# Optimization experiments

Hardware: AMD Instinct MI355X
Metric: run time of the kernel (lower is better)

Reference implementation:

```python
import jax, jax.numpy as jnp
import numpy as np

EMBED = 128          # embed_dim
HID = 128            # hidden_dim (must equal embed_dim for the view math to work)
HEADS = 4
HEAD_DIM = EMBED // HEADS  # = HID // HEADS = 32
N = 50000            # source cells
M = 50000            # target cells
E = 400000           # edges (nnz of inter_neighborhood)


def setup_inputs() -> dict:
    key = jax.random.key(0)
    ks = jax.random.split(key, 13)
    s = lambda d: 1.0 / np.sqrt(d)
    return {
        "source_features": jax.random.normal(ks[0], (N, EMBED), jnp.float32),
        "target_features": jax.random.normal(ks[1], (M, EMBED), jnp.float32),
        "edge_targets": jax.random.randint(ks[2], (E,), 0, M, dtype=jnp.int32),
        "edge_sources": jax.random.randint(ks[3], (E,), 0, N, dtype=jnp.int32),
        "Ws": jax.random.normal(ks[4], (EMBED, HEADS * HID), jnp.float32) * s(EMBED),
        "bs": jnp.zeros((HEADS * HID,), jnp.float32),
        "Wt": jax.random.normal(ks[5], (EMBED, HEADS * HID), jnp.float32) * s(EMBED),
        "bt": jnp.zeros((HEADS * HID,), jnp.float32),
        "attn_w": jax.random.normal(ks[6], (HEADS, HID), jnp.float32),
        "Wm": jax.random.normal(ks[7], (EMBED, EMBED), jnp.float32) * s(EMBED),
        "bm": jnp.zeros((EMBED,), jnp.float32),
        "Wo": jax.random.normal(ks[8], (EMBED, EMBED), jnp.float32) * s(EMBED),
        "bo": jnp.zeros((EMBED,), jnp.float32),
    }


def reference(source_features, target_features, edge_targets, edge_sources,
              Ws, bs, Wt, bt, attn_w, Wm, bm, Wo, bo):
    # Gather endpoint features per edge: [E, EMBED]
    src = source_features[edge_sources]
    tgt = target_features[edge_targets]
    # Fused linear + GELU attention hidden: [E, HEADS, HID]
    hidden = jax.nn.gelu((src @ Ws + bs) + (tgt @ Wt + bt), approximate=False)
    hidden = hidden.reshape(E, HEADS, HID)
    # Attention logits per edge/head: [E, HEADS]
    logits = jnp.einsum('ehd,hd->eh', hidden, attn_w)
    # Scatter-softmax over edges sharing the same target node
    mx = jax.ops.segment_max(logits, edge_targets, num_segments=M)
    ex = jnp.exp(logits - mx[edge_targets])
    den = jax.ops.segment_sum(ex, edge_targets, num_segments=M)
    scores = ex / den[edge_targets]                      # [E, HEADS]
    # Messages: [E, HEADS, HEAD_DIM], weighted and scatter-summed to targets
    msgs = (src @ Wm + bm).reshape(E, HEADS, HEAD_DIM) * scores[..., None]
    agg = jax.ops.segment_sum(msgs, edge_targets, num_segments=M)
    agg = agg.reshape(M, HEADS * HEAD_DIM)               # [M, EMBED]
    return agg @ Wo + bo
```

## Files before the change

### kernel.cpp

```cpp
#include <hip/hip_runtime.h>
#include <math.h>


typedef __bf16 bf16x8 __attribute__((ext_vector_type(8)));
typedef float  f32x4  __attribute__((ext_vector_type(4)));
typedef float  f32x2  __attribute__((ext_vector_type(2)));

__device__ __forceinline__ unsigned short f2bf(float x) {
    unsigned u = __float_as_uint(x);
    u += 0x7FFFu + ((u >> 16) & 1u);
    return (unsigned short)(u >> 16);
}
__device__ __forceinline__ float bf2f(unsigned short b) {
    return __uint_as_float(((unsigned)b) << 16);
}
__device__ __forceinline__ unsigned pack_tr(float a, float b) {
    return (__float_as_uint(a) >> 16) | (__float_as_uint(b) & 0xFFFF0000u);
}
__device__ __forceinline__ float res16(float x) {
    return x - __uint_as_float(__float_as_uint(x) & 0xFFFF0000u);
}
__device__ __forceinline__ unsigned short bf_rn(float x) {
    return (unsigned short)((__float_as_uint(x) + 0x8000u) >> 16);
}
__device__ __forceinline__ f32x2 up2(unsigned u) {
    f32x2 r;
    r.x = __uint_as_float(u << 16);
    r.y = __uint_as_float(u & 0xFFFF0000u);
    return r;
}
__device__ __forceinline__ float exp2_fast(float x) {
#if __has_builtin(__builtin_amdgcn_exp2f)
    return __builtin_amdgcn_exp2f(x);
#else
    return exp2f(x);
#endif
}

__device__ __forceinline__ f32x2 gelu2(f32x2 v) {
    f32x2 v2 = v * v;
    f32x2 u  = v * (v2 * 0.10294355f + 2.30220820f);
    f32x2 e;
    e.x = exp2_fast(u.x);
    e.y = exp2_fast(u.y);
    f32x2 r;
    r.x = __builtin_amdgcn_rcpf(e.x + 1.0f);
    r.y = __builtin_amdgcn_rcpf(e.y + 1.0f);
    return v - v * r;
}

__device__ __forceinline__ float edge_logit(uint4 h,
    f32x2 ht0, f32x2 ht1, f32x2 ht2, f32x2 ht3,
    f32x2 aw0, f32x2 aw1, f32x2 aw2, f32x2 aw3) {
    f32x2 qv = gelu2(up2(h.x) + ht0) * aw0;
    qv += gelu2(up2(h.y) + ht1) * aw1;
    qv += gelu2(up2(h.z) + ht2) * aw2;
    qv += gelu2(up2(h.w) + ht3) * aw3;
    return qv.x + qv.y;
}

__global__ __launch_bounds__(128)
void prep_weights_kernel(const float* __restrict__ Ws, const float* __restrict__ Wm,
                         const float* __restrict__ Wt, const float* __restrict__ Wo,
                         const float* __restrict__ bs, const float* __restrict__ bm,
                         unsigned short* __restrict__ WThi, unsigned short* __restrict__ WTlo,
                         float* __restrict__ bias_cat) {
    int n = blockIdx.x, k = threadIdx.x;
    float w;
    if      (n < 512)  w = Ws[(size_t)k * 512 + n];
    else if (n < 640)  w = Wm[(size_t)k * 128 + (n - 512)];
    else if (n < 1152) w = Wt[(size_t)k * 512 + (n - 640)];
    else               w = Wo[(size_t)k * 128 + (n - 1152)];
    unsigned short hi = f2bf(w);
    WThi[(size_t)n * 128 + k] = hi;
    WTlo[(size_t)n * 128 + k] = f2bf(w - bf2f(hi));
    if (k == 0 && n < 640) bias_cat[n] = (n < 512) ? bs[n] : bm[n - 512];
}

__global__ void hist_kernel(const int* __restrict__ tgt, int* __restrict__ counts, int E) {
    int e = blockIdx.x * blockDim.x + threadIdx.x;
    if (e < E) atomicAdd(&counts[tgt[e]], 1);
}

__global__ __launch_bounds__(256)
void scan_partial_kernel(const int* __restrict__ counts, int* __restrict__ partials, int M) {
    __shared__ int sdata[256];
    int b = blockIdx.x, tid = threadIdx.x;
    int base = b * 1024 + tid * 4;
    int s = 0;
#pragma unroll
    for (int k = 0; k < 4; ++k) { int idx = base + k; if (idx < M) s += counts[idx]; }
    sdata[tid] = s; __syncthreads();
    for (int d = 128; d > 0; d >>= 1) {
        if (tid < d) sdata[tid] += sdata[tid + d];
        __syncthreads();
    }
    if (tid == 0) partials[b] = sdata[0];
}

__global__ __launch_bounds__(64)
void scan_partials_kernel(const int* __restrict__ partials, int* __restrict__ pbase,
                          int* __restrict__ offsets, int P, int M) {
    int lane = threadIdx.x;
    int own = (lane < P) ? partials[lane] : 0;
    int v = own;
    for (int d = 1; d < 64; d <<= 1) {
        int o = __shfl_up(v, d);
        if (lane >= d) v += o;
    }
    if (lane < P) pbase[lane] = v - own;
    if (lane == 63) offsets[M] = v;
}

__global__ __launch_bounds__(256)
void scan_final_kernel(const int* __restrict__ counts, const int* __restrict__ pbase,
                       int* __restrict__ offsets, int M) {
    __shared__ int sdata[256];
    int b = blockIdx.x, tid = threadIdx.x;
    int base = b * 1024 + tid * 4;
    int c0 = 0, c1 = 0, c2 = 0, c3 = 0;
    if (base + 0 < M) c0 = counts[base + 0];
    if (base + 1 < M) c1 = counts[base + 1];
    if (base + 2 < M) c2 = counts[base + 2];
    if (base + 3 < M) c3 = counts[base + 3];
    int s = c0 + c1 + c2 + c3;
    sdata[tid] = s; __syncthreads();
    int v = s;
    for (int d = 1; d < 256; d <<= 1) {
        int o = (tid >= d) ? sdata[tid - d] : 0;
        __syncthreads();
        v += o;
        sdata[tid] = v;
        __syncthreads();
    }
    int ex = pbase[b] + v - s;
    if (base + 0 < M) offsets[base + 0] = ex;
    if (base + 1 < M) offsets[base + 1] = ex + c0;
    if (base + 2 < M) offsets[base + 2] = ex + c0 + c1;
    if (base + 3 < M) offsets[base + 3] = ex + c0 + c1 + c2;
}

__global__ void scatter_kernel(const int* __restrict__ tgt, const int* __restrict__ src,
                               const int* __restrict__ offsets,
                               int* __restrict__ cursor, int* __restrict__ srcs_sorted, int E) {
    int e = blockIdx.x * blockDim.x + threadIdx.x;
    if (e < E) {
        int t = tgt[e];
        int r = atomicAdd(&cursor[t], 1);
        srcs_sorted[offsets[t] + r] = src[e];
    }
}

__global__ __launch_bounds__(256, 3)
void gemm_hidden_kernel(const float* __restrict__ src_f, const float* __restrict__ tgt_f,
                        const unsigned short* __restrict__ WThi, const unsigned short* __restrict__ WTlo,
                        const float* __restrict__ bias_cat, const float* __restrict__ bt,
                        unsigned short* __restrict__ Hs, unsigned short* __restrict__ Hm,
                        unsigned short* __restrict__ Ht, int N, int M, int nT0) {
    __shared__ unsigned short BufHi[64 * 136];
    __shared__ unsigned short BufLo[64 * 136];

    int bx = blockIdx.x;
    bool side1 = bx >= nT0;
    const float* Af = side1 ? tgt_f : src_f;
    int rows = side1 ? M : N;
    int row0 = (side1 ? bx - nT0 : bx) * 64;
    int nCols = side1 ? 8 : 10;
    int colWbase = side1 ? 640 : 0;
    const float* bias = side1 ? bt : bias_cat;

    int tid = threadIdx.x;

#pragma unroll
    for (int l = 0; l < 4; ++l) {
        int idx = l * 256 + tid;
        int r = idx >> 4, c8 = idx & 15;
        int row = row0 + r;
        float4 v0 = make_float4(0.f, 0.f, 0.f, 0.f), v1 = v0;
        if (row < rows) {
            v0 = *(const float4*)(Af + (size_t)row * 128 + c8 * 8);
            v1 = *(const float4*)(Af + (size_t)row * 128 + c8 * 8 + 4);
        }
        uint4 hp, lp;
        hp.x = pack_tr(v0.x, v0.y); hp.y = pack_tr(v0.z, v0.w);
        hp.z = pack_tr(v1.x, v1.y); hp.w = pack_tr(v1.z, v1.w);
        lp.x = pack_tr(res16(v0.x), res16(v0.y)); lp.y = pack_tr(res16(v0.z), res16(v0.w));
        lp.z = pack_tr(res16(v1.x), res16(v1.y)); lp.w = pack_tr(res16(v1.z), res16(v1.w));
        *(uint4*)(&BufHi[r * 136 + c8 * 8]) = hp;
        *(uint4*)(&BufLo[r * 136 + c8 * 8]) = lp;
    }
    __syncthreads();

    int wid = tid >> 6, lane = tid & 63;
    int wm = (wid >> 1) * 32, wn = (wid & 1) * 32;
    int g = lane >> 4, r16 = lane & 15;

    bf16x8 Ah0[4], Ah1[4], Al0[4], Al1[4];
#pragma unroll
    for (int kk = 0; kk < 4; ++kk) {
        int k0 = kk * 32 + g * 8;
        Ah0[kk] = *(const bf16x8*)(&BufHi[(wm + r16) * 136 + k0]);
        Ah1[kk] = *(const bf16x8*)(&BufHi[(wm + 16 + r16) * 136 + k0]);
        Al0[kk] = *(const bf16x8*)(&BufLo[(wm + r16) * 136 + k0]);
        Al1[kk] = *(const bf16x8*)(&BufLo[(wm + 16 + r16) * 136 + k0]);
    }
    __syncthreads();

    for (int c = 0; c < nCols; ++c) {
        int colW = colWbase + c * 64;
#pragma unroll
        for (int l = 0; l < 4; ++l) {
            int ci = l * 256 + tid;
            int r = ci >> 4, c8 = ci & 15;
            uint4 vh = *(const uint4*)(WThi + (size_t)(colW + r) * 128 + c8 * 8);
            uint4 vl = *(const uint4*)(WTlo + (size_t)(colW + r) * 128 + c8 * 8);
            *(uint4*)(&BufHi[r * 136 + c8 * 8]) = vh;
            *(uint4*)(&BufLo[r * 136 + c8 * 8]) = vl;
        }
        __syncthreads();

        f32x4 acc00 = {0.f, 0.f, 0.f, 0.f}, acc01 = acc00, acc10 = acc00, acc11 = acc00;
#pragma unroll
        for (int kk = 0; kk < 4; ++kk) {
            int k0 = kk * 32 + g * 8;
            bf16x8 bh0 = *(const bf16x8*)(&BufHi[(wn + r16) * 136 + k0]);
            bf16x8 bh1 = *(const bf16x8*)(&BufHi[(wn + 16 + r16) * 136 + k0]);
            bf16x8 bl0 = *(const bf16x8*)(&BufLo[(wn + r16) * 136 + k0]);
            bf16x8 bl1 = *(const bf16x8*)(&BufLo[(wn + 16 + r16) * 136 + k0]);
            acc00 = __builtin_amdgcn_mfma_f32_16x16x32_bf16(Ah0[kk], bh0, acc00, 0, 0, 0);
            acc00 = __builtin_amdgcn_mfma_f32_16x16x32_bf16(Ah0[kk], bl0, acc00, 0, 0, 0);
            acc00 = __builtin_amdgcn_mfma_f32_16x16x32_bf16(Al0[kk], bh0, acc00, 0, 0, 0);
            acc01 = __builtin_amdgcn_mfma_f32_16x16x32_bf16(Ah0[kk], bh1, acc01, 0, 0, 0);
            acc01 = __builtin_amdgcn_mfma_f32_16x16x32_bf16(Ah0[kk], bl1, acc01, 0, 0, 0);
            acc01 = __builtin_amdgcn_mfma_f32_16x16x32_bf16(Al0[kk], bh1, acc01, 0, 0, 0);
            acc10 = __builtin_amdgcn_mfma_f32_16x16x32_bf16(Ah1[kk], bh0, acc10, 0, 0, 0);
            acc10 = __builtin_amdgcn_mfma_f32_16x16x32_bf16(Ah1[kk], bl0, acc10, 0, 0, 0);
            acc10 = __builtin_amdgcn_mfma_f32_16x16x32_bf16(Al1[kk], bh0, acc10, 0, 0, 0);
            acc11 = __builtin_amdgcn_mfma_f32_16x16x32_bf16(Ah1[kk], bh1, acc11, 0, 0, 0);
            acc11 = __builtin_amdgcn_mfma_f32_16x16x32_bf16(Ah1[kk], bl1, acc11, 0, 0, 0);
            acc11 = __builtin_amdgcn_mfma_f32_16x16x32_bf16(Al1[kk], bh1, acc11, 0, 0, 0);
        }

        int c0 = c * 64 + wn + r16;
        int c1 = c0 + 16;
        float bv0 = bias[c0], bv1 = bias[c1];
        unsigned short* out; int stride, oc0, oc1;
        if (side1)        { out = Ht; stride = 512; oc0 = c0;       oc1 = c1; }
        else if (c0 < 512){ out = Hs; stride = 512; oc0 = c0;       oc1 = c1; }
        else              { out = Hm; stride = 128; oc0 = c0 - 512; oc1 = c1 - 512; }
#pragma unroll
        for (int ii = 0; ii < 4; ++ii) {
            int rA = row0 + wm + g * 4 + ii;
            int rB = rA + 16;
            if (rA < rows) {
                out[(size_t)rA * stride + oc0] = bf_rn(acc00[ii] + bv0);
                out[(size_t)rA * stride + oc1] = bf_rn(acc01[ii] + bv1);
            }
            if (rB < rows) {
                out[(size_t)rB * stride + oc0] = bf_rn(acc10[ii] + bv0);
                out[(size_t)rB * stride + oc1] = bf_rn(acc11[ii] + bv1);
            }
        }
        __syncthreads();
    }
}

__global__ __launch_bounds__(256, 4)
void gemm_out_kernel(const unsigned short* __restrict__ A,
                     const unsigned short* __restrict__ BT,
                     const float* __restrict__ bias,
                     float* __restrict__ C, int Mrows, int Ntot) {
    __shared__ unsigned short As[64 * 136];
    __shared__ unsigned short Bs[64 * 136];
    int tid = threadIdx.x;
    int row0 = blockIdx.y * 64, col0 = blockIdx.x * 64;

#pragma unroll
    for (int l = 0; l < 4; ++l) {
        int idx = l * 256 + tid;
        int r = idx >> 4, c8 = idx & 15;
        int row = row0 + r;
        uint4 v = make_uint4(0, 0, 0, 0);
        if (row < Mrows) v = *(const uint4*)(A + (size_t)row * 128 + c8 * 8);
        *(uint4*)(&As[r * 136 + c8 * 8]) = v;
    }
#pragma unroll
    for (int l = 0; l < 4; ++l) {
        int idx = l * 256 + tid;
        int r = idx >> 4, c8 = idx & 15;
        uint4 v = *(const uint4*)(BT + (size_t)(col0 + r) * 128 + c8 * 8);
        *(uint4*)(&Bs[r * 136 + c8 * 8]) = v;
    }
    __syncthreads();

    int wid = tid >> 6, lane = tid & 63;
    int wm = (wid >> 1) * 32, wn = (wid & 1) * 32;
    int g = lane >> 4, r16 = lane & 15;

    f32x4 acc00 = {0.f, 0.f, 0.f, 0.f}, acc01 = acc00, acc10 = acc00, acc11 = acc00;

#pragma unroll
    for (int kk = 0; kk < 4; ++kk) {
        int k0 = kk * 32 + g * 8;
        bf16x8 a0 = *(const bf16x8*)(&As[(wm + r16) * 136 + k0]);
        bf16x8 a1 = *(const bf16x8*)(&As[(wm + 16 + r16) * 136 + k0]);
        bf16x8 b0 = *(const bf16x8*)(&Bs[(wn + r16) * 136 + k0]);
        bf16x8 b1 = *(const bf16x8*)(&Bs[(wn + 16 + r16) * 136 + k0]);
        acc00 = __builtin_amdgcn_mfma_f32_16x16x32_bf16(a0, b0, acc00, 0, 0, 0);
        acc01 = __builtin_amdgcn_mfma_f32_16x16x32_bf16(a0, b1, acc01, 0, 0, 0);
        acc10 = __builtin_amdgcn_mfma_f32_16x16x32_bf16(a1, b0, acc10, 0, 0, 0);
        acc11 = __builtin_amdgcn_mfma_f32_16x16x32_bf16(a1, b1, acc11, 0, 0, 0);
    }

    float bv0 = bias[col0 + wn + r16];
    float bv1 = bias[col0 + wn + 16 + r16];
#pragma unroll
    for (int i = 0; i < 4; ++i) {
        int rA = row0 + wm + g * 4 + i;
        int rB = rA + 16;
        if (rA < Mrows) {
            C[(size_t)rA * Ntot + col0 + wn + r16]      = acc00[i] + bv0;
            C[(size_t)rA * Ntot + col0 + wn + 16 + r16] = acc01[i] + bv1;
        }
        if (rB < Mrows) {
            C[(size_t)rB * Ntot + col0 + wn + r16]      = acc10[i] + bv0;
            C[(size_t)rB * Ntot + col0 + wn + 16 + r16] = acc11[i] + bv1;
        }
    }
}

__global__ __launch_bounds__(256)
void attn_kernel(const unsigned short* __restrict__ Hs, const unsigned short* __restrict__ Ht,
                 const unsigned short* __restrict__ Hm, const float* __restrict__ attn_w,
                 const int* __restrict__ offsets, const int* __restrict__ srcs,
                 unsigned short* __restrict__ agg, int M) {
    int wave = threadIdx.x >> 6;
    int lane = threadIdx.x & 63;
    int t = blockIdx.x * 4 + wave;
    if (t >= M) return;

    int j0 = lane << 3;
    uint4 h = *(const uint4*)(Ht + (size_t)t * 512 + j0);
    f32x2 ht0 = up2(h.x), ht1 = up2(h.y), ht2 = up2(h.z), ht3 = up2(h.w);
    const float L2E = 1.4426950408889634f;
    float4 a0 = *(const float4*)(attn_w + j0);
    float4 a1 = *(const float4*)(attn_w + j0 + 4);
    f32x2 aw0 = {a0.x * L2E, a0.y * L2E};
    f32x2 aw1 = {a0.z * L2E, a0.w * L2E};
    f32x2 aw2 = {a1.x * L2E, a1.y * L2E};
    f32x2 aw3 = {a1.z * L2E, a1.w * L2E};

    int off = offsets[t];
    int end = offsets[t + 1];
    int hm_off = lane << 1;

    float m = -INFINITY, den = 0.f;
    f32x2 acc = {0.f, 0.f};

    int i = off;
    uint4 hA, hB, hC, hD;
    unsigned mA, mB, mC, mD;
    bool have = (end - i) >= 4;
    if (have) {
        int s0 = srcs[i], s1 = srcs[i + 1], s2 = srcs[i + 2], s3 = srcs[i + 3];
        hA = *(const uint4*)(Hs + (size_t)s0 * 512 + j0);
        hB = *(const uint4*)(Hs + (size_t)s1 * 512 + j0);
        hC = *(const uint4*)(Hs + (size_t)s2 * 512 + j0);
        hD = *(const uint4*)(Hs + (size_t)s3 * 512 + j0);
        mA = *(const unsigned*)(Hm + (size_t)s0 * 128 + hm_off);
        mB = *(const unsigned*)(Hm + (size_t)s1 * 128 + hm_off);
        mC = *(const unsigned*)(Hm + (size_t)s2 * 128 + hm_off);
        mD = *(const unsigned*)(Hm + (size_t)s3 * 128 + hm_off);
    }
    while (have) {
        int ni = i + 4;
        bool nhave = (end - ni) >= 4;
        uint4 nhA, nhB, nhC, nhD;
        unsigned nmA, nmB, nmC, nmD;
        if (nhave) {
            int s0 = srcs[ni], s1 = srcs[ni + 1], s2 = srcs[ni + 2], s3 = srcs[ni + 3];
            nhA = *(const uint4*)(Hs + (size_t)s0 * 512 + j0);
            nhB = *(const uint4*)(Hs + (size_t)s1 * 512 + j0);
            nhC = *(const uint4*)(Hs + (size_t)s2 * 512 + j0);
            nhD = *(const uint4*)(Hs + (size_t)s3 * 512 + j0);
            nmA = *(const unsigned*)(Hm + (size_t)s0 * 128 + hm_off);
            nmB = *(const unsigned*)(Hm + (size_t)s1 * 128 + hm_off);
            nmC = *(const unsigned*)(Hm + (size_t)s2 * 128 + hm_off);
            nmD = *(const unsigned*)(Hm + (size_t)s3 * 128 + hm_off);
        }

        float q0 = edge_logit(hA, ht0, ht1, ht2, ht3, aw0, aw1, aw2, aw3);
        float q1 = edge_logit(hB, ht0, ht1, ht2, ht3, aw0, aw1, aw2, aw3);
        float q2 = edge_logit(hC, ht0, ht1, ht2, ht3, aw0, aw1, aw2, aw3);
        float q3 = edge_logit(hD, ht0, ht1, ht2, ht3, aw0, aw1, aw2, aw3);
        q0 += __shfl_xor(q0, 1); q1 += __shfl_xor(q1, 1); q2 += __shfl_xor(q2, 1); q3 += __shfl_xor(q3, 1);
        q0 += __shfl_xor(q0, 2); q1 += __shfl_xor(q1, 2); q2 += __shfl_xor(q2, 2); q3 += __shfl_xor(q3, 2);
        q0 += __shfl_xor(q0, 4); q1 += __shfl_xor(q1, 4); q2 += __shfl_xor(q2, 4); q3 += __shfl_xor(q3, 4);
        q0 += __shfl_xor(q0, 8); q1 += __shfl_xor(q1, 8); q2 += __shfl_xor(q2, 8); q3 += __shfl_xor(q3, 8);

        float nm = fmaxf(fmaxf(fmaxf(q0, q1), fmaxf(q2, q3)), m);
        float sc = exp2_fast(m - nm);
        float p0 = exp2_fast(q0 - nm);
        float p1 = exp2_fast(q1 - nm);
        float p2 = exp2_fast(q2 - nm);
        float p3 = exp2_fast(q3 - nm);
        den = fmaf(den, sc, (p0 + p1) + (p2 + p3));
        acc = acc * sc;
        acc += p0 * up2(mA);
        acc += p1 * up2(mB);
        acc += p2 * up2(mC);
        acc += p3 * up2(mD);
        m = nm;

        i = ni;
        if (nhave) {
            hA = nhA; hB = nhB; hC = nhC; hD = nhD;
            mA = nmA; mB = nmB; mC = nmC; mD = nmD;
        }
        have = nhave;
    }
    for (; i < end; ++i) {
        int s0 = srcs[i];
        uint4 hX = *(const uint4*)(Hs + (size_t)s0 * 512 + j0);
        unsigned mX = *(const unsigned*)(Hm + (size_t)s0 * 128 + hm_off);
        float q0 = edge_logit(hX, ht0, ht1, ht2, ht3, aw0, aw1, aw2, aw3);
        q0 += __shfl_xor(q0, 1);
        q0 += __shfl_xor(q0, 2);
        q0 += __shfl_xor(q0, 4);
        q0 += __shfl_xor(q0, 8);
        float nm = fmaxf(m, q0);
        float sc = exp2_fast(m - nm);
        float p0 = exp2_fast(q0 - nm);
        den = fmaf(den, sc, p0);
        acc = acc * sc + p0 * up2(mX);
        m = nm;
    }
    float r = (end > off) ? __builtin_amdgcn_rcpf(den) : 0.0f;
    ushort2 o;
    o.x = f2bf(acc.x * r);
    o.y = f2bf(acc.y * r);
    *(ushort2*)(agg + (size_t)t * 128 + hm_off) = o;
}

extern "C" void kernel_launch(void* const* d_in, const int* in_sizes, int n_in,
                              void* d_out, int out_size, void* d_ws, size_t ws_size,
                              hipStream_t stream) {
    const float* src_f  = (const float*)d_in[0];
    const float* tgt_f  = (const float*)d_in[1];
    const int*   e_tgt  = (const int*)d_in[2];
    const int*   e_src  = (const int*)d_in[3];
    const float* Ws     = (const float*)d_in[4];
    const float* bs     = (const float*)d_in[5];
    const float* Wt     = (const float*)d_in[6];
    const float* bt     = (const float*)d_in[7];
    const float* attn_w = (const float*)d_in[8];
    const float* Wm     = (const float*)d_in[9];
    const float* bm     = (const float*)d_in[10];
    const float* Wo     = (const float*)d_in[11];
    const float* bo     = (const float*)d_in[12];

    int N = in_sizes[0] / 128;
    int M = in_sizes[1] / 128;
    int E = in_sizes[2];

    char* ws = (char*)d_ws;
    size_t woff = 0;
    auto alloc = [&](size_t bytes) -> void* {
        void* p = ws + woff;
        woff += ((bytes + 255) / 256) * 256;
        return p;
    };
    unsigned short* Hs       = (unsigned short*)alloc((size_t)N * 512 * 2);
    unsigned short* Ht       = (unsigned short*)alloc((size_t)M * 512 * 2);
    unsigned short* Hm       = (unsigned short*)alloc((size_t)N * 128 * 2);
    unsigned short* agg_bf   = (unsigned short*)alloc((size_t)M * 128 * 2);
    unsigned short* WThi     = (unsigned short*)alloc((size_t)1280 * 128 * 2);
    unsigned short* WTlo     = (unsigned short*)alloc((size_t)1280 * 128 * 2);
    float*          bias_cat = (float*)alloc(640 * 4);
    int*            counts   = (int*)alloc((size_t)2 * M * 4);
    int*            cursor   = counts + M;
    int*            offsets  = (int*)alloc((size_t)(M + 1) * 4);
    int*            srcs     = (int*)alloc((size_t)E * 4);
    int*            partials = (int*)alloc(64 * 4);
    int*            pbase    = (int*)alloc(64 * 4);

    hipMemsetAsync(counts, 0, (size_t)2 * M * 4, stream);

    const int tb = 256;
    int P = (M + 1023) / 1024;

    hist_kernel<<<(E + tb - 1) / tb, tb, 0, stream>>>(e_tgt, counts, E);
    scan_partial_kernel<<<P, 256, 0, stream>>>(counts, partials, M);
    scan_partials_kernel<<<1, 64, 0, stream>>>(partials, pbase, offsets, P, M);
    scan_final_kernel<<<P, 256, 0, stream>>>(counts, pbase, offsets, M);
    scatter_kernel<<<(E + tb - 1) / tb, tb, 0, stream>>>(e_tgt, e_src, offsets, cursor, srcs, E);

    prep_weights_kernel<<<1280, 128, 0, stream>>>(Ws, Wm, Wt, Wo, bs, bm, WThi, WTlo, bias_cat);

    int nT0 = (N + 63) / 64, nT1 = (M + 63) / 64;
    gemm_hidden_kernel<<<nT0 + nT1, 256, 0, stream>>>(src_f, tgt_f, WThi, WTlo,
                                                      bias_cat, bt, Hs, Hm, Ht, N, M, nT0);

    attn_kernel<<<(M + 3) / 4, 256, 0, stream>>>(Hs, Ht, Hm, attn_w, offsets, srcs, agg_bf, M);

    dim3 go(128 / 64, (M + 63) / 64);
    gemm_out_kernel<<<go, 256, 0, stream>>>(agg_bf, WThi + (size_t)1152 * 128, bo,
                                            (float*)d_out, M, 128);
}
```

Measured before the change: 333.6 us.

## Prefetch weight tiles, split online softmax, share reciprocal in GELU

The hidden GEMM kernel now loads the next 64-column weight tile into registers while the current tile is consumed, overlapping global loads with MFMA work, and its launch bound rises to four blocks per CU. The edge attention kernel splits the online softmax into two independent running max/sum/accumulator chains that are merged after the loop, shortening the serial dependency. GELU computes one reciprocal for a pair of values by multiplying the two denominators. These add register pressure from the prefetch buffers and the extra occupancy target, and the shared reciprocal could overflow to inf when both exponentials are large.

```diff
diff --git a/kernel.cpp b/kernel.cpp
--- a/kernel.cpp
+++ b/kernel.cpp
@@ -40,12 +40,12 @@
 __device__ __forceinline__ f32x2 gelu2(f32x2 v) {
     f32x2 v2 = v * v;
     f32x2 u  = v * (v2 * 0.10294355f + 2.30220820f);
-    f32x2 e;
-    e.x = exp2_fast(u.x);
-    e.y = exp2_fast(u.y);
+    float ex = exp2_fast(u.x) + 1.0f;
+    float ey = exp2_fast(u.y) + 1.0f;
+    float rp = __builtin_amdgcn_rcpf(ex * ey);
     f32x2 r;
-    r.x = __builtin_amdgcn_rcpf(e.x + 1.0f);
-    r.y = __builtin_amdgcn_rcpf(e.y + 1.0f);
+    r.x = ey * rp;
+    r.y = ex * rp;
     return v - v * r;
 }
 
@@ -151,7 +151,7 @@
     }
 }
 
-__global__ __launch_bounds__(256, 3)
+__global__ __launch_bounds__(256, 4)
 void gemm_hidden_kernel(const float* __restrict__ src_f, const float* __restrict__ tgt_f,
                         const unsigned short* __restrict__ WThi, const unsigned short* __restrict__ WTlo,
                         const float* __restrict__ bias_cat, const float* __restrict__ bt,
@@ -206,18 +206,38 @@
     }
     __syncthreads();
 
-    for (int c = 0; c < nCols; ++c) {
-        int colW = colWbase + c * 64;
+    uint4 pbh[4], pbl[4];
+    {
+        int colW = colWbase;
 #pragma unroll
         for (int l = 0; l < 4; ++l) {
             int ci = l * 256 + tid;
             int r = ci >> 4, c8 = ci & 15;
-            uint4 vh = *(const uint4*)(WThi + (size_t)(colW + r) * 128 + c8 * 8);
-            uint4 vl = *(const uint4*)(WTlo + (size_t)(colW + r) * 128 + c8 * 8);
-            *(uint4*)(&BufHi[r * 136 + c8 * 8]) = vh;
-            *(uint4*)(&BufLo[r * 136 + c8 * 8]) = vl;
+            pbh[l] = *(const uint4*)(WThi + (size_t)(colW + r) * 128 + c8 * 8);
+            pbl[l] = *(const uint4*)(WTlo + (size_t)(colW + r) * 128 + c8 * 8);
+        }
+    }
+
+    for (int c = 0; c < nCols; ++c) {
+#pragma unroll
+        for (int l = 0; l < 4; ++l) {
+            int ci = l * 256 + tid;
+            int r = ci >> 4, c8 = ci & 15;
+            *(uint4*)(&BufHi[r * 136 + c8 * 8]) = pbh[l];
+            *(uint4*)(&BufLo[r * 136 + c8 * 8]) = pbl[l];
         }
         __syncthreads();
+
+        if (c + 1 < nCols) {
+            int colW = colWbase + (c + 1) * 64;
+#pragma unroll
+            for (int l = 0; l < 4; ++l) {
+                int ci = l * 256 + tid;
+                int r = ci >> 4, c8 = ci & 15;
+                pbh[l] = *(const uint4*)(WThi + (size_t)(colW + r) * 128 + c8 * 8);
+                pbl[l] = *(const uint4*)(WTlo + (size_t)(colW + r) * 128 + c8 * 8);
+            }
+        }
 
         f32x4 acc00 = {0.f, 0.f, 0.f, 0.f}, acc01 = acc00, acc10 = acc00, acc11 = acc00;
 #pragma unroll
@@ -354,8 +374,8 @@
     int end = offsets[t + 1];
     int hm_off = lane << 1;
 
-    float m = -INFINITY, den = 0.f;
-    f32x2 acc = {0.f, 0.f};
+    float m0 = -INFINITY, m1 = -INFINITY, den0 = 0.f, den1 = 0.f;
+    f32x2 ac0 = {0.f, 0.f}, ac1 = {0.f, 0.f};
 
     int i = off;
     uint4 hA, hB, hC, hD;
@@ -398,19 +418,24 @@
         q0 += __shfl_xor(q0, 4); q1 += __shfl_xor(q1, 4); q2 += __shfl_xor(q2, 4); q3 += __shfl_xor(q3, 4);
         q0 += __shfl_xor(q0, 8); q1 += __shfl_xor(q1, 8); q2 += __shfl_xor(q2, 8); q3 += __shfl_xor(q3, 8);
 
-        float nm = fmaxf(fmaxf(fmaxf(q0, q1), fmaxf(q2, q3)), m);
-        float sc = exp2_fast(m - nm);
-        float p0 = exp2_fast(q0 - nm);
-        float p1 = exp2_fast(q1 - nm);
-        float p2 = exp2_fast(q2 - nm);
-        float p3 = exp2_fast(q3 - nm);
-        den = fmaf(den, sc, (p0 + p1) + (p2 + p3));
-        acc = acc * sc;
-        acc += p0 * up2(mA);
-        acc += p1 * up2(mB);
-        acc += p2 * up2(mC);
-        acc += p3 * up2(mD);
-        m = nm;
+        float n0 = fmaxf(m0, fmaxf(q0, q1));
+        float s0c = exp2_fast(m0 - n0);
+        float p0 = exp2_fast(q0 - n0);
+        float p1 = exp2_fast(q1 - n0);
+        den0 = fmaf(den0, s0c, p0 + p1);
+        ac0 = ac0 * s0c;
+        ac0 += p0 * up2(mA);
+        ac0 += p1 * up2(mB);
+        m0 = n0;
+        float n1 = fmaxf(m1, fmaxf(q2, q3));
+        float s1c = exp2_fast(m1 - n1);
+        float p2 = exp2_fast(q2 - n1);
+        float p3 = exp2_fast(q3 - n1);
+        den1 = fmaf(den1, s1c, p2 + p3);
+        ac1 = ac1 * s1c;
+        ac1 += p2 * up2(mC);
+        ac1 += p3 * up2(mD);
+        m1 = n1;
 
         i = ni;
         if (nhave) {
@@ -418,6 +443,14 @@
             mA = nmA; mB = nmB; mC = nmC; mD = nmD;
         }
         have = nhave;
+    }
+    if (m1 != -INFINITY) {
+        float mm = fmaxf(m0, m1);
+        float s0c = exp2_fast(m0 - mm);
+        float s1c = exp2_fast(m1 - mm);
+        den0 = den0 * s0c + den1 * s1c;
+        ac0 = ac0 * s0c + ac1 * s1c;
+        m0 = mm;
     }
     for (; i < end; ++i) {
         int s0 = srcs[i];
@@ -428,17 +461,17 @@
         q0 += __shfl_xor(q0, 2);
         q0 += __shfl_xor(q0, 4);
         q0 += __shfl_xor(q0, 8);
-        float nm = fmaxf(m, q0);
-        float sc = exp2_fast(m - nm);
+        float nm = fmaxf(m0, q0);
+        float sc = exp2_fast(m0 - nm);
         float p0 = exp2_fast(q0 - nm);
-        den = fmaf(den, sc, p0);
-        acc = acc * sc + p0 * up2(mX);
-        m = nm;
-    }
-    float r = (end > off) ? __builtin_amdgcn_rcpf(den) : 0.0f;
+        den0 = fmaf(den0, sc, p0);
+        ac0 = ac0 * sc + p0 * up2(mX);
+        m0 = nm;
+    }
+    float r = (end > off) ? __builtin_amdgcn_rcpf(den0) : 0.0f;
     ushort2 o;
-    o.x = f2bf(acc.x * r);
-    o.y = f2bf(acc.y * r);
+    o.x = f2bf(ac0.x * r);
+    o.y = f2bf(ac0.y * r);
     *(ushort2*)(agg + (size_t)t * 128 + hm_off) = o;
 }
 
```

New measurement: 460.1 us. 37.9% more time.
